# Kernel tuning notes

Hardware: AMD Instinct MI355X
Metric: run time of the kernel (lower is better)

The kernel has to match this reference:

```python
import jax, jax.numpy as jnp
import numpy as np

N_NODES = 100000
N_EDGES = 400000
N_GRAPHS = 2000
NODE_F = 78
HID = 128


def gcn_conv(x, src, dst, W, b, n_nodes):
    # PyG GCNConv: h = X @ W; add self-loops; symmetric norm; scatter-add; + bias
    h = x @ W
    loop = jnp.arange(n_nodes, dtype=src.dtype)
    s = jnp.concatenate([src, loop])
    d = jnp.concatenate([dst, loop])
    deg = jax.ops.segment_sum(jnp.ones_like(d, dtype=h.dtype), d, num_segments=n_nodes)
    dinv = jax.lax.rsqrt(deg)  # deg >= 1 due to self-loops
    coef = dinv[s] * dinv[d]  # [E+N]
    msg = h[s] * coef[:, None]  # gather + scale
    out = jax.ops.segment_sum(msg, d, num_segments=n_nodes)
    return out + b


def setup_inputs() -> dict:
    key = jax.random.key(0)
    ks = jax.random.split(key, 16)
    x = jax.random.normal(ks[0], (N_NODES, NODE_F), dtype=jnp.float32)
    edge_index = jax.random.randint(ks[1], (2, N_EDGES), 0, N_NODES, dtype=jnp.int64)
    batch = jnp.sort(jax.random.randint(ks[2], (N_NODES,), 0, N_GRAPHS, dtype=jnp.int64))
    def lin(k, fi, fo):
        lim = 1.0 / np.sqrt(fi)
        kw, kb = jax.random.split(k)
        return (jax.random.uniform(kw, (fi, fo), jnp.float32, -lim, lim),
                jax.random.uniform(kb, (fo,), jnp.float32, -lim, lim))
    W1, b1 = lin(ks[3], NODE_F, HID)
    W2, b2 = lin(ks[4], HID, 2 * HID)
    W3, b3 = lin(ks[5], 2 * HID, HID)
    fw1, fb1 = lin(ks[6], HID, 64)
    fw2, fb2 = lin(ks[7], 64, 1)
    return {"x": x, "edge_index": edge_index, "batch": batch,
            "W1": W1, "b1": b1, "W2": W2, "b2": b2, "W3": W3, "b3": b3,
            "fw1": fw1, "fb1": fb1, "fw2": fw2, "fb2": fb2}


def reference(x, edge_index, batch, W1, b1, W2, b2, W3, b3, fw1, fb1, fw2, fb2):
    src, dst = edge_index[0], edge_index[1]
    h = jax.nn.relu(gcn_conv(x, src, dst, W1, b1, N_NODES))
    h = jax.nn.relu(gcn_conv(h, src, dst, W2, b2, N_NODES))
    h = jax.nn.relu(gcn_conv(h, src, dst, W3, b3, N_NODES))
    # global_mean_pool over graph ids
    sums = jax.ops.segment_sum(h, batch, num_segments=N_GRAPHS)
    cnts = jax.ops.segment_sum(jnp.ones((N_NODES,), h.dtype), batch, num_segments=N_GRAPHS)
    pooled = sums / jnp.maximum(cnts, 1.0)[:, None]
    h = jax.nn.relu(pooled @ fw1 + fb1)
    return h @ fw2 + fb2  # [N_GRAPHS, 1]
```

## Files before the change

kernel.cpp:

```cpp
#include <hip/hip_runtime.h>

#define N_NODES 100000
#define N_EDGES 400000
#define N_GRAPHS 2000
#define NODE_F 78
#define HID 128
#define PAD 32
#define SENT N_NODES

typedef __attribute__((ext_vector_type(8))) short short8v;
typedef __attribute__((ext_vector_type(4))) float f32x4;

__device__ __forceinline__ ushort f2bf(float f) {
    unsigned u = __float_as_uint(f);
    unsigned r = (u + 0x7FFFu + ((u >> 16) & 1u)) >> 16;
    return (ushort)r;
}
__device__ __forceinline__ float bf2f(ushort b) {
    return __uint_as_float(((unsigned)b) << 16);
}
__device__ __forceinline__ float2 bfx2(const ushort* p) {
    unsigned u = *reinterpret_cast<const unsigned*>(p);
    return make_float2(__uint_as_float(u << 16), __uint_as_float(u & 0xffff0000u));
}
__device__ __forceinline__ unsigned packbf(float a, float b) {
    return (unsigned)f2bf(a) | ((unsigned)f2bf(b) << 16);
}


__global__ void setup_k(int* __restrict__ cursor, int4* __restrict__ csr4,
                        ushort* __restrict__ xb, ushort* __restrict__ b1,
                        ushort* __restrict__ b3) {
    int i = blockIdx.x * blockDim.x + threadIdx.x;
    if (i < N_NODES * PAD / 4) csr4[i] = make_int4(SENT, SENT, SENT, SENT);
    if (i < N_NODES) cursor[i] = 0;
    if (i < 80) xb[(size_t)N_NODES * 80 + i] = 0;
    if (i < 128) {
        b1[(size_t)N_NODES * 128 + i] = 0;
        b3[(size_t)N_NODES * 128 + i] = 0;
    }
}

__global__ void fill_csr_k(const int* __restrict__ src, const int* __restrict__ dst,
                           int* __restrict__ cursor, int* __restrict__ csr) {
    int e = blockIdx.x * blockDim.x + threadIdx.x;
    if (e >= N_EDGES) return;
    int s = src[e], d = dst[e];
    int p = atomicAdd(&cursor[d], 1);
    if (p < PAD) csr[d * PAD + p] = s;
}

__global__ void dinv_k(const int* __restrict__ deg, float* __restrict__ dinv, int n) {
    int i = blockIdx.x * blockDim.x + threadIdx.x;
    if (i < n) dinv[i] = rsqrtf((float)deg[i] + 1.0f);
}


__global__ void x2bf_k(const float* __restrict__ x, const float* __restrict__ dinv,
                       ushort* __restrict__ xb) {
    int idx = blockIdx.x * blockDim.x + threadIdx.x;
    if (idx >= N_NODES * 80) return;
    int n = idx / 80, f = idx - n * 80;
    xb[idx] = (f < NODE_F) ? f2bf(x[(long long)n * NODE_F + f] * dinv[n]) : (ushort)0;
}


__global__ void prep_wt_k(const float* __restrict__ W, ushort* __restrict__ Wth,
                          int K, int N) {
    int idx = blockIdx.x * blockDim.x + threadIdx.x;
    if (idx >= N * 256) return;
    int n = idx >> 8, k = idx & 255;
    Wth[idx] = (k < K) ? f2bf(W[(long long)k * N + n]) : (ushort)0;
}


__global__ __launch_bounds__(256) void gemm1_k(
        const ushort* __restrict__ A, int M,
        const ushort* __restrict__ Wth, const float* __restrict__ bias,
        const float* __restrict__ dinv, ushort* __restrict__ C) {
    __shared__ ushort At[128 * 64];
    __shared__ ushort Bh[128 * 64];
    const int tid = threadIdx.x;
    const int w = tid >> 6, l = tid & 63;
    const int bm = blockIdx.x * 128;

    f32x4 acc[2][8];
    #pragma unroll
    for (int m = 0; m < 2; ++m)
        #pragma unroll
        for (int j = 0; j < 8; ++j)
            acc[m][j] = (f32x4){0.f, 0.f, 0.f, 0.f};

    for (int k0 = 0; k0 < 128; k0 += 64) {
        __syncthreads();
        #pragma unroll
        for (int i = 0; i < 4; ++i) {
            int idx = tid + i * 256;
            int r = idx >> 3, s0 = idx & 7;
            int gr = bm + r; if (gr >= M) gr = M - 1;
            int kk = k0 + s0 * 8;
            short8v v;
            if (kk < 80) v = *reinterpret_cast<const short8v*>(&A[(size_t)gr * 80 + kk]);
            else v = (short8v){0,0,0,0,0,0,0,0};
            *reinterpret_cast<short8v*>(&At[r * 64 + (s0 ^ (r & 7)) * 8]) = v;
        }
        #pragma unroll
        for (int i = 0; i < 4; ++i) {
            int idx = tid + i * 256;
            int n = idx >> 3, s0 = idx & 7;
            long long g = (long long)n * 256 + k0 + s0 * 8;
            *reinterpret_cast<short8v*>(&Bh[n * 64 + (s0 ^ (n & 7)) * 8]) =
                *reinterpret_cast<const short8v*>(&Wth[g]);
        }
        __syncthreads();
        #pragma unroll
        for (int ks = 0; ks < 2; ++ks) {
            short8v ah[2];
            #pragma unroll
            for (int m = 0; m < 2; ++m) {
                int r = w * 32 + m * 16 + (l & 15);
                ah[m] = *reinterpret_cast<const short8v*>(
                    &At[r * 64 + ((ks * 4 + (l >> 4)) ^ (r & 7)) * 8]);
            }
            #pragma unroll
            for (int j = 0; j < 8; ++j) {
                int n = j * 16 + (l & 15);
                short8v bh = *reinterpret_cast<const short8v*>(
                    &Bh[n * 64 + ((ks * 4 + (l >> 4)) ^ (n & 7)) * 8]);
                #pragma unroll
                for (int m = 0; m < 2; ++m)
                    acc[m][j] = __builtin_amdgcn_mfma_f32_16x16x32_bf16(ah[m], bh, acc[m][j], 0, 0, 0);
            }
        }
    }

    float dv[2][4];
    #pragma unroll
    for (int m = 0; m < 2; ++m)
        #pragma unroll
        for (int rg = 0; rg < 4; ++rg) {
            int gr = bm + w * 32 + m * 16 + (l >> 4) * 4 + rg;
            dv[m][rg] = (gr < M) ? dinv[gr] : 0.f;
        }
    #pragma unroll
    for (int j = 0; j < 8; ++j) {
        int gc = j * 16 + (l & 15);
        float bv = bias[gc];
        #pragma unroll
        for (int m = 0; m < 2; ++m) {
            #pragma unroll
            for (int rg = 0; rg < 4; ++rg) {
                int gr = bm + w * 32 + m * 16 + (l >> 4) * 4 + rg;
                if (gr < M)
                    C[(size_t)gr * 128 + gc] = f2bf(fmaxf(acc[m][j][rg] + bv, 0.0f) * dv[m][rg]);
            }
        }
    }
}


__global__ __launch_bounds__(512) void gemm23_k(
        const ushort* __restrict__ A,
        const ushort* __restrict__ W2h, const float* __restrict__ b2,
        const ushort* __restrict__ W3h, const float* __restrict__ dinv,
        ushort* __restrict__ C, int M) {
    __shared__ ushort At[128 * 64];
    __shared__ ushort Bh[128 * 64];
    const int tid = threadIdx.x;
    const int w = tid >> 6, l = tid & 63;
    const int bm = blockIdx.x * 128;

    f32x4 acc2[16];
    #pragma unroll
    for (int j = 0; j < 16; ++j) acc2[j] = (f32x4){0.f, 0.f, 0.f, 0.f};

    for (int k0 = 0; k0 < 128; k0 += 64) {
        __syncthreads();
        #pragma unroll
        for (int i = 0; i < 2; ++i) {
            int idx = tid + i * 512;
            int r = idx >> 3, s0 = idx & 7;
            int gr = bm + r; if (gr >= M) gr = M - 1;
            *reinterpret_cast<short8v*>(&At[r * 64 + (s0 ^ (r & 7)) * 8]) =
                *reinterpret_cast<const short8v*>(&A[(size_t)gr * 128 + k0 + s0 * 8]);
        }
        #pragma unroll
        for (int nh = 0; nh < 2; ++nh) {
            if (nh) __syncthreads();
            #pragma unroll
            for (int i = 0; i < 2; ++i) {
                int idx = tid + i * 512;
                int n = idx >> 3, s0 = idx & 7;
                long long g = (long long)(nh * 128 + n) * 256 + k0 + s0 * 8;
                *reinterpret_cast<short8v*>(&Bh[n * 64 + (s0 ^ (n & 7)) * 8]) =
                    *reinterpret_cast<const short8v*>(&W2h[g]);
            }
            __syncthreads();
            #pragma unroll
            for (int ks = 0; ks < 2; ++ks) {
                int r = w * 16 + (l & 15);
                short8v ah = *reinterpret_cast<const short8v*>(
                    &At[r * 64 + ((ks * 4 + (l >> 4)) ^ (r & 7)) * 8]);
                #pragma unroll
                for (int jl = 0; jl < 8; ++jl) {
                    int n = jl * 16 + (l & 15);
                    short8v bh = *reinterpret_cast<const short8v*>(
                        &Bh[n * 64 + ((ks * 4 + (l >> 4)) ^ (n & 7)) * 8]);
                    acc2[nh * 8 + jl] = __builtin_amdgcn_mfma_f32_16x16x32_bf16(ah, bh, acc2[nh * 8 + jl], 0, 0, 0);
                }
            }
        }
    }

    f32x4 acc3[8];
    #pragma unroll
    for (int j = 0; j < 8; ++j) acc3[j] = (f32x4){0.f, 0.f, 0.f, 0.f};

    #pragma unroll
    for (int ch = 0; ch < 4; ++ch) {
        __syncthreads();
        #pragma unroll
        for (int jj = 0; jj < 4; ++jj) {
            int j = ch * 4 + jj;
            float bv = b2[j * 16 + (l & 15)];
            #pragma unroll
            for (int rg = 0; rg < 4; ++rg) {
                int r = w * 16 + (l >> 4) * 4 + rg;
                int cl = jj * 16 + (l & 15);
                At[r * 64 + ((cl >> 3) ^ (r & 7)) * 8 + (cl & 7)] =
                    f2bf(fmaxf(acc2[j][rg] + bv, 0.f));
            }
        }
        #pragma unroll
        for (int i = 0; i < 2; ++i) {
            int idx = tid + i * 512;
            int n = idx >> 3, s0 = idx & 7;
            long long g = (long long)n * 256 + ch * 64 + s0 * 8;
            *reinterpret_cast<short8v*>(&Bh[n * 64 + (s0 ^ (n & 7)) * 8]) =
                *reinterpret_cast<const short8v*>(&W3h[g]);
        }
        __syncthreads();
        #pragma unroll
        for (int ks = 0; ks < 2; ++ks) {
            int r = w * 16 + (l & 15);
            short8v ah = *reinterpret_cast<const short8v*>(
                &At[r * 64 + ((ks * 4 + (l >> 4)) ^ (r & 7)) * 8]);
            #pragma unroll
            for (int j3 = 0; j3 < 8; ++j3) {
                int n = j3 * 16 + (l & 15);
                short8v bh = *reinterpret_cast<const short8v*>(
                    &Bh[n * 64 + ((ks * 4 + (l >> 4)) ^ (n & 7)) * 8]);
                acc3[j3] = __builtin_amdgcn_mfma_f32_16x16x32_bf16(ah, bh, acc3[j3], 0, 0, 0);
            }
        }
    }

    float dv[4];
    #pragma unroll
    for (int rg = 0; rg < 4; ++rg) {
        int gr = bm + w * 16 + (l >> 4) * 4 + rg;
        dv[rg] = (gr < M) ? dinv[gr] : 0.f;
    }
    #pragma unroll
    for (int j = 0; j < 8; ++j) {
        int gc = j * 16 + (l & 15);
        #pragma unroll
        for (int rg = 0; rg < 4; ++rg) {
            int gr = bm + w * 16 + (l >> 4) * 4 + rg;
            if (gr < M) C[(size_t)gr * 128 + gc] = f2bf(acc3[j][rg] * dv[rg]);
        }
    }
}


__global__ __launch_bounds__(256) void gather78_k(const ushort* __restrict__ Xb,
        const int* __restrict__ deg, const int* __restrict__ csr,
        const float* __restrict__ dinv, ushort* __restrict__ out) {
    int wid = (blockIdx.x * blockDim.x + threadIdx.x) >> 6;
    int lane = threadIdx.x & 63;
    if (wid >= N_NODES) return;
    float di = dinv[wid];
    float ax = 0.f, ay = 0.f;
    bool act = lane < 40;
    if (act) {
        float2 v = bfx2(&Xb[(size_t)wid * 80 + lane * 2]);
        ax = v.x; ay = v.y;
    }
    int d = deg[wid]; if (d > PAD) d = PAD;
    const int4* e4 = reinterpret_cast<const int4*>(csr + wid * PAD);
    for (int j0 = 0; j0 < d; j0 += 4) {
        int4 e = e4[j0 >> 2];
        if (act) {
            float2 v0 = bfx2(&Xb[(size_t)e.x * 80 + lane * 2]);
            float2 v1 = bfx2(&Xb[(size_t)e.y * 80 + lane * 2]);
            float2 v2 = bfx2(&Xb[(size_t)e.z * 80 + lane * 2]);
            float2 v3 = bfx2(&Xb[(size_t)e.w * 80 + lane * 2]);
            ax += v0.x + v1.x + v2.x + v3.x;
            ay += v0.y + v1.y + v2.y + v3.y;
        }
    }
    if (act)
        *reinterpret_cast<unsigned*>(&out[(size_t)wid * 80 + lane * 2]) = packbf(ax * di, ay * di);
}

__global__ __launch_bounds__(256) void gather128_k(const ushort* __restrict__ A,
        const int* __restrict__ deg, const int* __restrict__ csr,
        const float* __restrict__ dinv, ushort* __restrict__ out) {
    int wid = (blockIdx.x * blockDim.x + threadIdx.x) >> 6;
    int lane = threadIdx.x & 63;
    if (wid >= N_NODES) return;
    float di = dinv[wid];
    float2 v = bfx2(&A[(size_t)wid * 128 + lane * 2]);
    float ax = v.x, ay = v.y;
    int d = deg[wid]; if (d > PAD) d = PAD;
    const int4* e4 = reinterpret_cast<const int4*>(csr + wid * PAD);
    for (int j0 = 0; j0 < d; j0 += 4) {
        int4 e = e4[j0 >> 2];
        float2 w0 = bfx2(&A[(size_t)e.x * 128 + lane * 2]);
        float2 w1 = bfx2(&A[(size_t)e.y * 128 + lane * 2]);
        float2 w2 = bfx2(&A[(size_t)e.z * 128 + lane * 2]);
        float2 w3 = bfx2(&A[(size_t)e.w * 128 + lane * 2]);
        ax += w0.x + w1.x + w2.x + w3.x;
        ay += w0.y + w1.y + w2.y + w3.y;
    }
    *reinterpret_cast<unsigned*>(&out[(size_t)wid * 128 + lane * 2]) = packbf(ax * di, ay * di);
}


__global__ __launch_bounds__(512) void pool_head_k(
        const ushort* __restrict__ A,
        const int* __restrict__ deg, const int* __restrict__ csr,
        const float* __restrict__ dinv, const float* __restrict__ b3,
        const int* __restrict__ batch,
        const float* __restrict__ fw1, const float* __restrict__ fb1,
        const float* __restrict__ fw2, const float* __restrict__ fb2,
        float* __restrict__ out) {
    __shared__ float part[8][HID];
    __shared__ float ps[HID];
    const int g = blockIdx.x;
    const int w = threadIdx.x >> 6, lane = threadIdx.x & 63;

    int start, end;
    {
        int l = 0, h = N_NODES;
        while (l < h) { int m = (l + h) >> 1; if (batch[m] < g) l = m + 1; else h = m; }
        start = l;
        h = N_NODES;
        while (l < h) { int m = (l + h) >> 1; if (batch[m] < g + 1) l = m + 1; else h = m; }
        end = l;
    }

    float sx = 0.f, sy = 0.f;
    const float bx = b3[lane * 2], by = b3[lane * 2 + 1];
    for (int i = start + w; i < end; i += 8) {
        float di = dinv[i];
        float2 v = bfx2(&A[(size_t)i * 128 + lane * 2]);
        float ax = v.x, ay = v.y;
        int d = deg[i]; if (d > PAD) d = PAD;
        const int4* e4 = reinterpret_cast<const int4*>(csr + i * PAD);
        for (int j0 = 0; j0 < d; j0 += 4) {
            int4 e = e4[j0 >> 2];
            float2 w0 = bfx2(&A[(size_t)e.x * 128 + lane * 2]);
            float2 w1 = bfx2(&A[(size_t)e.y * 128 + lane * 2]);
            float2 w2 = bfx2(&A[(size_t)e.z * 128 + lane * 2]);
            float2 w3 = bfx2(&A[(size_t)e.w * 128 + lane * 2]);
            ax += w0.x + w1.x + w2.x + w3.x;
            ay += w0.y + w1.y + w2.y + w3.y;
        }
        sx += fmaxf(ax * di + bx, 0.f);
        sy += fmaxf(ay * di + by, 0.f);
    }
    part[w][lane * 2] = sx;
    part[w][lane * 2 + 1] = sy;
    __syncthreads();

    if (w == 0) {
        float inv = (end > start) ? 1.0f / (float)(end - start) : 0.0f;
        float s0 = 0.f, s1 = 0.f;
        #pragma unroll
        for (int q = 0; q < 8; ++q) {
            s0 += part[q][lane * 2];
            s1 += part[q][lane * 2 + 1];
        }
        ps[lane * 2] = s0 * inv;
        ps[lane * 2 + 1] = s1 * inv;
    }
    __syncthreads();

    if (w == 0) {
        float acc = fb1[lane];
        #pragma unroll 8
        for (int k = 0; k < HID; ++k) acc = fmaf(ps[k], fw1[k * 64 + lane], acc);
        float v = fmaxf(acc, 0.0f) * fw2[lane];
        #pragma unroll
        for (int off = 32; off > 0; off >>= 1) v += __shfl_down(v, off);
        if (lane == 0) out[g] = v + fb2[0];
    }
}


extern "C" void kernel_launch(void* const* d_in, const int* in_sizes, int n_in,
                              void* d_out, int out_size, void* d_ws, size_t ws_size,
                              hipStream_t stream) {
    const float* x     = (const float*)d_in[0];
    const int*   ei    = (const int*)d_in[1];
    const int*   batch = (const int*)d_in[2];
    const float* W1 = (const float*)d_in[3];
    const float* b1 = (const float*)d_in[4];
    const float* W2 = (const float*)d_in[5];
    const float* b2 = (const float*)d_in[6];
    const float* W3 = (const float*)d_in[7];
    const float* b3 = (const float*)d_in[8];
    const float* fw1 = (const float*)d_in[9];
    const float* fb1 = (const float*)d_in[10];
    const float* fw2 = (const float*)d_in[11];
    const float* fb2 = (const float*)d_in[12];
    float* out = (float*)d_out;

    const int* src = ei;
    const int* dst = ei + N_EDGES;

    char* p = (char*)d_ws;
    float*  dinv  = (float*)p;  p += 100352 * 4;
    int*    cur   = (int*)p;    p += 100352 * 4;
    int*    csr   = (int*)p;    p += (size_t)N_NODES * PAD * 4;
    ushort* w1h   = (ushort*)p; p += 256 * 256 * 2;
    ushort* w2h   = (ushort*)p; p += 256 * 256 * 2;
    ushort* w3h   = (ushort*)p; p += 256 * 256 * 2;
    ushort* xb    = (ushort*)p; p += (size_t)(N_NODES + 1) * 80 * 2;
    ushort* xpadb = (ushort*)p; p += (size_t)N_NODES * 80 * 2;
    ushort* buf1  = (ushort*)p; p += (size_t)(N_NODES + 1) * 128 * 2;
    ushort* buf2  = (ushort*)p; p += (size_t)N_NODES * 128 * 2;
    ushort* buf3  = (ushort*)p; p += (size_t)(N_NODES + 1) * 128 * 2;

    const int T = 256;
    const int gw = (N_NODES * 64 + T - 1) / T;

    setup_k<<<(N_NODES * PAD / 4 + T - 1) / T, T, 0, stream>>>(cur, (int4*)csr, xb, buf1, buf3);
    fill_csr_k<<<(N_EDGES + T - 1) / T, T, 0, stream>>>(src, dst, cur, csr);
    dinv_k<<<(N_NODES + T - 1) / T, T, 0, stream>>>(cur, dinv, N_NODES);
    x2bf_k<<<(N_NODES * 80 + T - 1) / T, T, 0, stream>>>(x, dinv, xb);

    prep_wt_k<<<(128 * 256 + T - 1) / T, T, 0, stream>>>(W1, w1h, NODE_F, 128);
    prep_wt_k<<<(256 * 256 + T - 1) / T, T, 0, stream>>>(W2, w2h, HID, 256);
    prep_wt_k<<<(128 * 256 + T - 1) / T, T, 0, stream>>>(W3, w3h, 2 * HID, 128);

    gather78_k<<<gw, T, 0, stream>>>(xb, cur, csr, dinv, xpadb);
    gemm1_k<<<782, 256, 0, stream>>>(xpadb, N_NODES, w1h, b1, dinv, buf1);

    gather128_k<<<gw, T, 0, stream>>>(buf1, cur, csr, dinv, buf2);
    gemm23_k<<<782, 512, 0, stream>>>(buf2, w2h, b2, w3h, dinv, buf3, N_NODES);

    pool_head_k<<<N_GRAPHS, 512, 0, stream>>>(buf3, cur, csr, dinv, b3, batch,
                                              fw1, fb1, fw2, fb2, out);
}
```

Measured before the change: 327.0 us.

## Stream pre-swizzled weight images into LDS with async double-buffered global_load_lds

The gather kernel now writes its output in the XOR-swizzled LDS layout, and W2/W3 are pre-packed into swizzled LDS images. This lets gemm23 copy A and weight tiles straight into shared memory with global_load_lds. Weight chunks are double-buffered so the next chunk loads while MFMAs run, and each wave's layer-3 input tile now lives in a private LDS buffer. The goal is to remove register-staged loads and extra barriers, at the cost of more LDS per block, which may lower occupancy. The last block reads past the end of buf2 with no row clamp.

After: 308.9 us. 5.5% less time.

```diff
diff --git a/kernel.cpp b/kernel.cpp
--- a/kernel.cpp
+++ b/kernel.cpp
@@ -25,6 +25,10 @@
 }
 __device__ __forceinline__ unsigned packbf(float a, float b) {
     return (unsigned)f2bf(a) | ((unsigned)f2bf(b) << 16);
+}
+__device__ __forceinline__ void gload16(const ushort* g, ushort* l) {
+    __builtin_amdgcn_global_load_lds((const __attribute__((address_space(1))) unsigned int*)g,
+                                     (__attribute__((address_space(3))) unsigned int*)l, 16, 0, 0);
 }
 
 
@@ -73,6 +77,23 @@
     Wth[idx] = (k < K) ? f2bf(W[(long long)k * N + n]) : (ushort)0;
 }
 
+__global__ void prep_w2img_k(const float* __restrict__ W2, ushort* __restrict__ img) {
+    int idx = blockIdx.x * blockDim.x + threadIdx.x;
+    if (idx >= 256 * 128) return;
+    int n = idx >> 7, k = idx & 127;
+    int c = k >> 3;
+    int slot = (c & 8) | ((c & 7) ^ (n & 7));
+    img[n * 128 + slot * 8 + (k & 7)] = f2bf(W2[(long long)k * 256 + n]);
+}
+
+__global__ void prep_w3img_k(const float* __restrict__ W3, ushort* __restrict__ img) {
+    int idx = blockIdx.x * blockDim.x + threadIdx.x;
+    if (idx >= 128 * 256) return;
+    int n = idx >> 8, k = idx & 255;
+    int ch = k >> 6, cc = (k >> 3) & 7;
+    img[ch * 8192 + n * 64 + ((cc ^ (n & 7)) * 8) + (k & 7)] = f2bf(W3[(long long)k * 128 + n]);
+}
+
 
 __global__ __launch_bounds__(256) void gemm1_k(
         const ushort* __restrict__ A, int M,
@@ -161,98 +182,101 @@
 
 __global__ __launch_bounds__(512) void gemm23_k(
         const ushort* __restrict__ A,
-        const ushort* __restrict__ W2h, const float* __restrict__ b2,
-        const ushort* __restrict__ W3h, const float* __restrict__ dinv,
+        const ushort* __restrict__ W2i, const float* __restrict__ b2,
+        const ushort* __restrict__ W3i, const float* __restrict__ dinv,
         ushort* __restrict__ C, int M) {
-    __shared__ ushort At[128 * 64];
-    __shared__ ushort Bh[128 * 64];
+    __shared__ ushort At[128 * 128];
+    __shared__ ushort Wb[2][8192];
+    __shared__ ushort Tb[8][1024];
     const int tid = threadIdx.x;
     const int w = tid >> 6, l = tid & 63;
     const int bm = blockIdx.x * 128;
 
+    {
+        const ushort* asrc = A + (size_t)bm * 128;
+        #pragma unroll
+        for (int i = 0; i < 4; ++i) {
+            int chunk = w * 4 + i;
+            gload16(asrc + chunk * 512 + l * 8, &At[chunk * 512]);
+        }
+        #pragma unroll
+        for (int i = 0; i < 2; ++i) {
+            int chunk = w * 2 + i;
+            gload16(W2i + chunk * 512 + l * 8, &Wb[0][chunk * 512]);
+        }
+    }
+    __syncthreads();
+
     f32x4 acc2[16];
     #pragma unroll
     for (int j = 0; j < 16; ++j) acc2[j] = (f32x4){0.f, 0.f, 0.f, 0.f};
 
-    for (int k0 = 0; k0 < 128; k0 += 64) {
+    #pragma unroll
+    for (int q = 0; q < 4; ++q) {
+        const ushort* nsrc = (q < 3) ? (W2i + (q + 1) * 8192) : W3i;
+        #pragma unroll
+        for (int i = 0; i < 2; ++i) {
+            int chunk = w * 2 + i;
+            gload16(nsrc + chunk * 512 + l * 8, &Wb[(q + 1) & 1][chunk * 512]);
+        }
+        const ushort* wb = Wb[q & 1];
+        #pragma unroll
+        for (int ks = 0; ks < 4; ++ks) {
+            int r = w * 16 + (l & 15);
+            int ck = ks * 4 + (l >> 4);
+            int sa = (ck & 8) | ((ck & 7) ^ (r & 7));
+            short8v ah = *reinterpret_cast<const short8v*>(&At[r * 128 + sa * 8]);
+            #pragma unroll
+            for (int jt = 0; jt < 4; ++jt) {
+                int n = jt * 16 + (l & 15);
+                int sb = (ck & 8) | ((ck & 7) ^ (n & 7));
+                short8v bh = *reinterpret_cast<const short8v*>(&wb[n * 128 + sb * 8]);
+                acc2[q * 4 + jt] = __builtin_amdgcn_mfma_f32_16x16x32_bf16(ah, bh, acc2[q * 4 + jt], 0, 0, 0);
+            }
+        }
         __syncthreads();
-        #pragma unroll
-        for (int i = 0; i < 2; ++i) {
-            int idx = tid + i * 512;
-            int r = idx >> 3, s0 = idx & 7;
-            int gr = bm + r; if (gr >= M) gr = M - 1;
-            *reinterpret_cast<short8v*>(&At[r * 64 + (s0 ^ (r & 7)) * 8]) =
-                *reinterpret_cast<const short8v*>(&A[(size_t)gr * 128 + k0 + s0 * 8]);
-        }
-        #pragma unroll
-        for (int nh = 0; nh < 2; ++nh) {
-            if (nh) __syncthreads();
+    }
+
+    f32x4 acc3[8];
+    #pragma unroll
+    for (int j = 0; j < 8; ++j) acc3[j] = (f32x4){0.f, 0.f, 0.f, 0.f};
+
+    #pragma unroll
+    for (int ch = 0; ch < 4; ++ch) {
+        if (ch < 3) {
+            const ushort* nsrc = W3i + (ch + 1) * 8192;
             #pragma unroll
             for (int i = 0; i < 2; ++i) {
-                int idx = tid + i * 512;
-                int n = idx >> 3, s0 = idx & 7;
-                long long g = (long long)(nh * 128 + n) * 256 + k0 + s0 * 8;
-                *reinterpret_cast<short8v*>(&Bh[n * 64 + (s0 ^ (n & 7)) * 8]) =
-                    *reinterpret_cast<const short8v*>(&W2h[g]);
-            }
-            __syncthreads();
-            #pragma unroll
-            for (int ks = 0; ks < 2; ++ks) {
-                int r = w * 16 + (l & 15);
-                short8v ah = *reinterpret_cast<const short8v*>(
-                    &At[r * 64 + ((ks * 4 + (l >> 4)) ^ (r & 7)) * 8]);
-                #pragma unroll
-                for (int jl = 0; jl < 8; ++jl) {
-                    int n = jl * 16 + (l & 15);
-                    short8v bh = *reinterpret_cast<const short8v*>(
-                        &Bh[n * 64 + ((ks * 4 + (l >> 4)) ^ (n & 7)) * 8]);
-                    acc2[nh * 8 + jl] = __builtin_amdgcn_mfma_f32_16x16x32_bf16(ah, bh, acc2[nh * 8 + jl], 0, 0, 0);
-                }
-            }
-        }
-    }
-
-    f32x4 acc3[8];
-    #pragma unroll
-    for (int j = 0; j < 8; ++j) acc3[j] = (f32x4){0.f, 0.f, 0.f, 0.f};
-
-    #pragma unroll
-    for (int ch = 0; ch < 4; ++ch) {
-        __syncthreads();
+                int chunk = w * 2 + i;
+                gload16(nsrc + chunk * 512 + l * 8, &Wb[(ch + 1) & 1][chunk * 512]);
+            }
+        }
         #pragma unroll
         for (int jj = 0; jj < 4; ++jj) {
             int j = ch * 4 + jj;
-            float bv = b2[j * 16 + (l & 15)];
+            float bv = b2[ch * 64 + jj * 16 + (l & 15)];
             #pragma unroll
             for (int rg = 0; rg < 4; ++rg) {
-                int r = w * 16 + (l >> 4) * 4 + rg;
+                int rr = (l >> 4) * 4 + rg;
                 int cl = jj * 16 + (l & 15);
-                At[r * 64 + ((cl >> 3) ^ (r & 7)) * 8 + (cl & 7)] =
+                Tb[w][rr * 64 + (((cl >> 3) ^ (rr & 7)) * 8) + (cl & 7)] =
                     f2bf(fmaxf(acc2[j][rg] + bv, 0.f));
             }
         }
-        #pragma unroll
-        for (int i = 0; i < 2; ++i) {
-            int idx = tid + i * 512;
-            int n = idx >> 3, s0 = idx & 7;
-            long long g = (long long)n * 256 + ch * 64 + s0 * 8;
-            *reinterpret_cast<short8v*>(&Bh[n * 64 + (s0 ^ (n & 7)) * 8]) =
-                *reinterpret_cast<const short8v*>(&W3h[g]);
-        }
-        __syncthreads();
+        const ushort* wb = Wb[ch & 1];
         #pragma unroll
         for (int ks = 0; ks < 2; ++ks) {
-            int r = w * 16 + (l & 15);
-            short8v ah = *reinterpret_cast<const short8v*>(
-                &At[r * 64 + ((ks * 4 + (l >> 4)) ^ (r & 7)) * 8]);
+            int rt = l & 15;
+            int ck = ks * 4 + (l >> 4);
+            short8v ah = *reinterpret_cast<const short8v*>(&Tb[w][rt * 64 + ((ck ^ (rt & 7)) * 8)]);
             #pragma unroll
             for (int j3 = 0; j3 < 8; ++j3) {
                 int n = j3 * 16 + (l & 15);
-                short8v bh = *reinterpret_cast<const short8v*>(
-                    &Bh[n * 64 + ((ks * 4 + (l >> 4)) ^ (n & 7)) * 8]);
+                short8v bh = *reinterpret_cast<const short8v*>(&wb[n * 64 + ((ck ^ (n & 7)) * 8)]);
                 acc3[j3] = __builtin_amdgcn_mfma_f32_16x16x32_bf16(ah, bh, acc3[j3], 0, 0, 0);
             }
         }
+        __syncthreads();
     }
 
     float dv[4];
@@ -323,7 +347,9 @@
         ax += w0.x + w1.x + w2.x + w3.x;
         ay += w0.y + w1.y + w2.y + w3.y;
     }
-    *reinterpret_cast<unsigned*>(&out[(size_t)wid * 128 + lane * 2]) = packbf(ax * di, ay * di);
+    int kt = lane >> 5, cc = (lane >> 2) & 7, q4 = lane & 3;
+    int slot = kt * 8 + (cc ^ (wid & 7));
+    *reinterpret_cast<unsigned*>(&out[(size_t)wid * 128 + slot * 8 + q4 * 2]) = packbf(ax * di, ay * di);
 }
 
 
@@ -425,8 +451,8 @@
     int*    cur   = (int*)p;    p += 100352 * 4;
     int*    csr   = (int*)p;    p += (size_t)N_NODES * PAD * 4;
     ushort* w1h   = (ushort*)p; p += 256 * 256 * 2;
-    ushort* w2h   = (ushort*)p; p += 256 * 256 * 2;
-    ushort* w3h   = (ushort*)p; p += 256 * 256 * 2;
+    ushort* img2  = (ushort*)p; p += 256 * 128 * 2;
+    ushort* img3  = (ushort*)p; p += 128 * 256 * 2;
     ushort* xb    = (ushort*)p; p += (size_t)(N_NODES + 1) * 80 * 2;
     ushort* xpadb = (ushort*)p; p += (size_t)N_NODES * 80 * 2;
     ushort* buf1  = (ushort*)p; p += (size_t)(N_NODES + 1) * 128 * 2;
@@ -442,14 +468,14 @@
     x2bf_k<<<(N_NODES * 80 + T - 1) / T, T, 0, stream>>>(x, dinv, xb);
 
     prep_wt_k<<<(128 * 256 + T - 1) / T, T, 0, stream>>>(W1, w1h, NODE_F, 128);
-    prep_wt_k<<<(256 * 256 + T - 1) / T, T, 0, stream>>>(W2, w2h, HID, 256);
-    prep_wt_k<<<(128 * 256 + T - 1) / T, T, 0, stream>>>(W3, w3h, 2 * HID, 128);
+    prep_w2img_k<<<(256 * 128 + T - 1) / T, T, 0, stream>>>(W2, img2);
+    prep_w3img_k<<<(128 * 256 + T - 1) / T, T, 0, stream>>>(W3, img3);
 
     gather78_k<<<gw, T, 0, stream>>>(xb, cur, csr, dinv, xpadb);
     gemm1_k<<<782, 256, 0, stream>>>(xpadb, N_NODES, w1h, b1, dinv, buf1);
 
     gather128_k<<<gw, T, 0, stream>>>(buf1, cur, csr, dinv, buf2);
-    gemm23_k<<<782, 512, 0, stream>>>(buf2, w2h, b2, w3h, dinv, buf3, N_NODES);
+    gemm23_k<<<782, 512, 0, stream>>>(buf2, img2, b2, img3, dinv, buf3, N_NODES);
 
     pool_head_k<<<N_GRAPHS, 512, 0, stream>>>(buf3, cur, csr, dinv, b3, batch,
                                               fw1, fb1, fw2, fb2, out);
```
